# Performance work log

Hardware: AMD Instinct MI355X
Metric: run time of the kernel (lower is better)

The kernel has to match this reference:

```python
import jax, jax.numpy as jnp
import numpy as np

# --- module hyperparameters (from init_kwargs) ---
IN_FEATURES = 256
TAU_MIN = 1.0
TAU_MAX = 20.0
K = 4
ALPHA = 1.0
NTAU = 100
SEQ_LEN = 2048
N_S = NTAU + 2 * K  # 108 taustars including k padding on both sides


def _laplace_constants():
    # c = (tau_max/tau_min)**(1/(ntau-1)) - 1
    c = (TAU_MAX / TAU_MIN) ** (1.0 / (NTAU - 1)) - 1.0
    tau_star = TAU_MIN * (1.0 + c) ** jnp.arange(-K, NTAU + K, dtype=jnp.float32)  # (N_S,)
    s = K / tau_star                      # (N_S,) decay rates
    e_s = jnp.exp(-s)                     # (N_S,)
    return s, e_s


def setup_inputs() -> dict:
    key = jax.random.key(0)
    inp = jax.random.normal(key, (SEQ_LEN, IN_FEATURES), dtype=jnp.float32)
    return {"inp": inp}


def reference(inp):
    """Laplace transform forward: diagonal linear recurrence over time.

    inp: (T, F) -> out: (T, N_S, F)
    t_n = e_alph_dur * t_{n-1} + decay * inp_n,  t_0 = 0
    """
    s, e_s = _laplace_constants()
    dur = TAU_MIN
    alpha = ALPHA
    e_alph_dur = e_s ** (dur * alpha)          # (N_S,)
    decay = (1.0 - e_alph_dur) / s             # (N_S,)

    # tIN[n, i, f] = decay[i] * inp[n, f]  -- matches matmul((N_S,1),(T,1,F))
    tIN = decay[None, :, None] * inp[:, None, :]   # (T, N_S, F)

    def step(t, x):
        t_new = e_alph_dur[:, None] * t + x
        return t_new, t_new

    t0 = jnp.zeros((N_S, inp.shape[1]), dtype=inp.dtype)
    _, out = jax.lax.scan(step, t0, tIN)       # (T, N_S, F)
    return out
```

## Files before the change

### kernel.cpp

```cpp
#include <hip/hip_runtime.h>


#define T_LEN 2048
#define F_DIM 256
#define NS    108
#define KPAD  4
#define CH    32
#define NB    (T_LEN / CH)

#define STATE_FLOATS ((size_t)NB * NS * 64 * 4)

typedef float f32x4 __attribute__((ext_vector_type(4)));

__device__ __forceinline__ void laplace_consts(int i, float& s, float& e, float& decay) {
    const float c   = powf(20.0f, 1.0f / 99.0f) - 1.0f;
    const float tau = powf(1.0f + c, (float)(i - KPAD));
    s     = 4.0f / tau;
    e     = expf(-s);
    decay = (1.0f - e) / s;
}

__device__ __forceinline__ size_t ws_idx(int b, int i, int lane) {
    return (((size_t)b * NS + i) * 64 + lane) * 4;
}

__global__ __launch_bounds__(128) void laplace_init(float* __restrict__ tab) {
    const int i = threadIdx.x;
    if (i < NS) {
        float s, e, d;
        laplace_consts(i, s, e, d);
        tab[i]          = e;
        tab[NS + i]     = d;
        tab[2 * NS + i] = expf(-s * (float)CH);
    }
}

__global__ __launch_bounds__(256) void laplace_local(
    const float* __restrict__ inp,
    float* __restrict__ ws,
    const float* __restrict__ tab)
{
    const int lane = threadIdx.x & 63;
    const int i    = blockIdx.y * 4 + (threadIdx.x >> 6);
    const int b    = blockIdx.x;

    const float e = tab[i];
    const float d = tab[NS + i];

    const float* ip = inp + lane * 4;
    float t0 = 0.f, t1 = 0.f, t2 = 0.f, t3 = 0.f;

    const int n0 = b * CH;
    #pragma unroll 8
    for (int n = n0; n < n0 + CH; ++n) {
        f32x4 x = *(const f32x4*)(ip + (size_t)n * F_DIM);
        t0 = fmaf(e, t0, d * x.x);
        t1 = fmaf(e, t1, d * x.y);
        t2 = fmaf(e, t2, d * x.z);
        t3 = fmaf(e, t3, d * x.w);
    }
    f32x4 r; r.x = t0; r.y = t1; r.z = t2; r.w = t3;
    *(f32x4*)(ws + ws_idx(b, i, lane)) = r;
}

__global__ __launch_bounds__(256) void laplace_combine(
    float* __restrict__ ws,
    const float* __restrict__ tab)
{
    const int lane = threadIdx.x & 63;
    const int i    = blockIdx.x * 4 + (threadIdx.x >> 6);

    const float g = tab[2 * NS + i];

    float S0 = 0.f, S1 = 0.f, S2 = 0.f, S3 = 0.f;
    #pragma unroll 8
    for (int b = 0; b < NB; ++b) {
        f32x4* p = (f32x4*)(ws + ws_idx(b, i, lane));
        f32x4 L = *p;
        f32x4 S; S.x = S0; S.y = S1; S.z = S2; S.w = S3;
        *p = S;
        S0 = fmaf(g, S0, L.x);
        S1 = fmaf(g, S1, L.y);
        S2 = fmaf(g, S2, L.z);
        S3 = fmaf(g, S3, L.w);
    }
}

__global__ __launch_bounds__(256) void laplace_burst(
    const float* __restrict__ inp,
    const float* __restrict__ ws,
    const float* __restrict__ tab,
    float* __restrict__ out)
{
    __shared__ float xs[CH][F_DIM];

    const int tid  = threadIdx.x;
    const int w    = tid >> 6;
    const int lane = tid & 63;
    const int f0   = lane * 4;
    const int ig   = blockIdx.x;
    const int b    = blockIdx.y;
    const int i    = ig * 4 + w;
    const int n0   = b * CH;

    const float e = tab[i];
    const float d = tab[NS + i];

    const float* ip = inp + (size_t)n0 * F_DIM + f0;
    f32x4 v[8];
    #pragma unroll
    for (int r = 0; r < 8; ++r)
        v[r] = *(const f32x4*)(ip + (size_t)(w * 8 + r) * F_DIM);

    f32x4 S = *(const f32x4*)(ws + ws_idx(b, i, lane));

    #pragma unroll
    for (int r = 0; r < 8; ++r)
        *(f32x4*)(&xs[w * 8 + r][f0]) = v[r];
    __syncthreads();

    float t0 = S.x, t1 = S.y, t2 = S.z, t3 = S.w;
    float* op = out + (size_t)n0 * (NS * F_DIM) + (size_t)i * F_DIM + f0;

    #pragma unroll 8
    for (int n = 0; n < CH; ++n) {
        f32x4 x = *(const f32x4*)(&xs[n][f0]);
        t0 = fmaf(e, t0, d * x.x);
        t1 = fmaf(e, t1, d * x.y);
        t2 = fmaf(e, t2, d * x.z);
        t3 = fmaf(e, t3, d * x.w);
        f32x4 r; r.x = t0; r.y = t1; r.z = t2; r.w = t3;
        __builtin_nontemporal_store(r, (f32x4*)(op + (size_t)n * (NS * F_DIM)));
    }
}

#define CHUNK_FB 64
#define WARM_FB  48
__global__ __launch_bounds__(256) void laplace_kernel_fb(
    const float* __restrict__ inp,
    float* __restrict__ out)
{
    const int tid  = threadIdx.x;
    const int lane = tid & 63;
    const int f0   = lane * 4;
    const int i    = blockIdx.y * 4 + (tid >> 6);
    const int n0   = blockIdx.x * CHUNK_FB;

    float s, e, decay;
    laplace_consts(i, s, e, decay);

    const float* ip = inp + f0;
    float t0 = 0.f, t1 = 0.f, t2 = 0.f, t3 = 0.f;

    int nstart = n0 - WARM_FB;
    if (nstart < 0) nstart = 0;
    #pragma unroll 4
    for (int n = nstart; n < n0; ++n) {
        f32x4 x = *(const f32x4*)(ip + (size_t)n * F_DIM);
        t0 = fmaf(e, t0, decay * x.x);
        t1 = fmaf(e, t1, decay * x.y);
        t2 = fmaf(e, t2, decay * x.z);
        t3 = fmaf(e, t3, decay * x.w);
    }
    float* op = out + (size_t)i * F_DIM + f0;
    #pragma unroll 4
    for (int n = n0; n < n0 + CHUNK_FB; ++n) {
        f32x4 x = *(const f32x4*)(ip + (size_t)n * F_DIM);
        t0 = fmaf(e, t0, decay * x.x);
        t1 = fmaf(e, t1, decay * x.y);
        t2 = fmaf(e, t2, decay * x.z);
        t3 = fmaf(e, t3, decay * x.w);
        f32x4 r; r.x = t0; r.y = t1; r.z = t2; r.w = t3;
        *(f32x4*)(op + (size_t)n * (NS * F_DIM)) = r;
    }
}

extern "C" void kernel_launch(void* const* d_in, const int* in_sizes, int n_in,
                              void* d_out, int out_size, void* d_ws, size_t ws_size,
                              hipStream_t stream) {
    const float* inp = (const float*)d_in[0];
    float* out = (float*)d_out;

    const size_t ws_need = (STATE_FLOATS + 3 * NS) * sizeof(float);

    if (d_ws != nullptr && ws_size >= ws_need) {
        float* ws  = (float*)d_ws;
        float* tab = ws + STATE_FLOATS;
        laplace_init   <<<dim3(1),          128, 0, stream>>>(tab);
        laplace_local  <<<dim3(NB, NS / 4), 256, 0, stream>>>(inp, ws, tab);
        laplace_combine<<<dim3(NS / 4),     256, 0, stream>>>(ws, tab);
        laplace_burst  <<<dim3(NS / 4, NB), 256, 0, stream>>>(inp, ws, tab, out);
    } else {
        laplace_kernel_fb<<<dim3(T_LEN / CHUNK_FB, NS / 4), 256, 0, stream>>>(inp, out);
    }
}
```

Before: 246.3 us.

## Restructure burst kernel so each block writes contiguous full timestep slices

The final output kernel is reorganised so each block owns 4 timesteps and all 108 taustars. Each wave carries 27 state vectors in registers, warm-started from the 32-step chunk prefix by replaying up to 28 steps. Every block then writes contiguous 108x256 slabs of the output with ordinary stores instead of strided nontemporal stores. This trades redundant recurrence work (warm-up replay) and high register pressure for better write locality and a grid of 512 blocks.

```diff
diff --git a/kernel.cpp b/kernel.cpp
--- a/kernel.cpp
+++ b/kernel.cpp
@@ -7,6 +7,9 @@
 #define KPAD  4
 #define CH    32
 #define NB    (T_LEN / CH)
+#define CHC   4
+#define NBC   (T_LEN / CHC)
+#define NJ    27
 
 #define STATE_FLOATS ((size_t)NB * NS * 64 * 4)
 
@@ -22,6 +25,10 @@
 
 __device__ __forceinline__ size_t ws_idx(int b, int i, int lane) {
     return (((size_t)b * NS + i) * 64 + lane) * 4;
+}
+
+__device__ __forceinline__ float sgpr_bcast(float x) {
+    return __int_as_float(__builtin_amdgcn_readfirstlane(__float_as_int(x)));
 }
 
 __global__ __launch_bounds__(128) void laplace_init(float* __restrict__ tab) {
@@ -86,7 +93,7 @@
     }
 }
 
-__global__ __launch_bounds__(256) void laplace_burst(
+__global__ __launch_bounds__(256) void laplace_slice2(
     const float* __restrict__ inp,
     const float* __restrict__ ws,
     const float* __restrict__ tab,
@@ -98,39 +105,58 @@
     const int w    = tid >> 6;
     const int lane = tid & 63;
     const int f0   = lane * 4;
-    const int ig   = blockIdx.x;
-    const int b    = blockIdx.y;
-    const int i    = ig * 4 + w;
-    const int n0   = b * CH;
-
-    const float e = tab[i];
-    const float d = tab[NS + i];
-
-    const float* ip = inp + (size_t)n0 * F_DIM + f0;
+    const int b2   = blockIdx.x;
+    const int n0   = b2 * CHC;
+    const int b32  = n0 >> 5;
+    const int base = b32 * CH;
+    const int warm = n0 - base;
+
+    const float* ip = inp + (size_t)base * F_DIM + f0;
     f32x4 v[8];
     #pragma unroll
     for (int r = 0; r < 8; ++r)
         v[r] = *(const f32x4*)(ip + (size_t)(w * 8 + r) * F_DIM);
-
-    f32x4 S = *(const f32x4*)(ws + ws_idx(b, i, lane));
-
     #pragma unroll
     for (int r = 0; r < 8; ++r)
         *(f32x4*)(&xs[w * 8 + r][f0]) = v[r];
+
+    float eS[NJ], dS[NJ];
+    #pragma unroll
+    for (int k = 0; k < NJ; ++k) {
+        eS[k] = sgpr_bcast(tab[4 * k + w]);
+        dS[k] = sgpr_bcast(tab[NS + 4 * k + w]);
+    }
+
+    f32x4 st[NJ];
+    #pragma unroll
+    for (int k = 0; k < NJ; ++k)
+        st[k] = *(const f32x4*)(ws + ws_idx(b32, 4 * k + w, lane));
+
     __syncthreads();
 
-    float t0 = S.x, t1 = S.y, t2 = S.z, t3 = S.w;
-    float* op = out + (size_t)n0 * (NS * F_DIM) + (size_t)i * F_DIM + f0;
-
-    #pragma unroll 8
-    for (int n = 0; n < CH; ++n) {
+    for (int n = 0; n < warm; ++n) {
         f32x4 x = *(const f32x4*)(&xs[n][f0]);
-        t0 = fmaf(e, t0, d * x.x);
-        t1 = fmaf(e, t1, d * x.y);
-        t2 = fmaf(e, t2, d * x.z);
-        t3 = fmaf(e, t3, d * x.w);
-        f32x4 r; r.x = t0; r.y = t1; r.z = t2; r.w = t3;
-        __builtin_nontemporal_store(r, (f32x4*)(op + (size_t)n * (NS * F_DIM)));
+        #pragma unroll
+        for (int k = 0; k < NJ; ++k) {
+            st[k].x = fmaf(eS[k], st[k].x, dS[k] * x.x);
+            st[k].y = fmaf(eS[k], st[k].y, dS[k] * x.y);
+            st[k].z = fmaf(eS[k], st[k].z, dS[k] * x.z);
+            st[k].w = fmaf(eS[k], st[k].w, dS[k] * x.w);
+        }
+    }
+
+    #pragma unroll
+    for (int n = 0; n < CHC; ++n) {
+        f32x4 x = *(const f32x4*)(&xs[warm + n][f0]);
+        float* op = out + (size_t)(n0 + n) * (NS * F_DIM) + tid * 4;
+        #pragma unroll
+        for (int k = 0; k < NJ; ++k) {
+            st[k].x = fmaf(eS[k], st[k].x, dS[k] * x.x);
+            st[k].y = fmaf(eS[k], st[k].y, dS[k] * x.y);
+            st[k].z = fmaf(eS[k], st[k].z, dS[k] * x.z);
+            st[k].w = fmaf(eS[k], st[k].w, dS[k] * x.w);
+            *(f32x4*)(op + (size_t)k * 1024) = st[k];
+        }
     }
 }
 
@@ -189,7 +215,7 @@
         laplace_init   <<<dim3(1),          128, 0, stream>>>(tab);
         laplace_local  <<<dim3(NB, NS / 4), 256, 0, stream>>>(inp, ws, tab);
         laplace_combine<<<dim3(NS / 4),     256, 0, stream>>>(ws, tab);
-        laplace_burst  <<<dim3(NS / 4, NB), 256, 0, stream>>>(inp, ws, tab, out);
+        laplace_slice2 <<<dim3(NBC),        256, 0, stream>>>(inp, ws, tab, out);
     } else {
         laplace_kernel_fb<<<dim3(T_LEN / CHUNK_FB, NS / 4), 256, 0, stream>>>(inp, out);
     }
```

New measurement: 255.7 us. 1.04x slower.
